# Kernel tuning notes

Measured on AMD Instinct MI355X. Metric: run time of the kernel, lower is better.

The kernel has to match this reference:

```python
import jax, jax.numpy as jnp
import numpy as np

N_NODES = 646  # fixed by nn.LayerNorm([646, 64])
LN_EPS = 1e-5


def gcn_conv(x, edge_index, W, b):
    """PyG GCNConv: out = D^-1/2 (A+I) D^-1/2 (x W) + b, scatter-add at target."""
    n = x.shape[0]
    h = x @ W  # [N, out_dim]
    loop = jnp.arange(n, dtype=edge_index.dtype)
    row = jnp.concatenate([edge_index[0], loop])  # source
    col = jnp.concatenate([edge_index[1], loop])  # target
    deg = jax.ops.segment_sum(jnp.ones_like(col, dtype=h.dtype), col, num_segments=n)
    dinv = jnp.where(deg > 0, jax.lax.rsqrt(deg), 0.0)
    norm = dinv[row] * dinv[col]  # [E+N]
    out = jax.ops.segment_sum(h[row] * norm[:, None], col, num_segments=n)
    return out + b


def setup_inputs() -> dict:
    key = jax.random.key(0)
    ks = jax.random.split(key, 8)
    F, H, L, E = 32768, 64, 128, 646 * 64
    x = jax.random.normal(ks[0], (N_NODES, F), dtype=jnp.float32)
    edge_index = jax.random.randint(ks[1], (2, E), 0, N_NODES, dtype=jnp.int64)
    s = 1.0 / np.sqrt(F)
    W1 = jax.random.normal(ks[2], (F, H), dtype=jnp.float32) * s
    b1 = jax.random.normal(ks[3], (H,), dtype=jnp.float32) * 0.01
    W2 = jax.random.normal(ks[4], (H, L), dtype=jnp.float32) * (1.0 / np.sqrt(H))
    b2 = jax.random.normal(ks[5], (L,), dtype=jnp.float32) * 0.01
    LPw = jax.random.normal(ks[6], (F, H), dtype=jnp.float32) * s
    LPb = jax.random.normal(ks[7], (H,), dtype=jnp.float32) * 0.01
    return {"x": x, "edge_index": edge_index, "W1": W1, "b1": b1,
            "W2": W2, "b2": b2, "LPw": LPw, "LPb": LPb}


def reference(x, edge_index, W1, b1, W2, b2, LPw, LPb):
    res = x @ LPw + LPb                       # Linear residual branch [N, 64]
    h = gcn_conv(x, edge_index, W1, b1)       # GCN1 [N, 64]
    h = res + h
    h = h * jax.nn.sigmoid(h)                 # SiLU
    # LayerNorm over BOTH dims [646, 64], no affine (elementwise_affine=False)
    mu = jnp.mean(h)
    var = jnp.mean(jnp.square(h - mu))
    h = (h - mu) * jax.lax.rsqrt(var + LN_EPS)
    out = gcn_conv(h, edge_index, W2, b2)     # GCN2 [N, num_label]
    return out
```

## Files before the change

kernel.cpp:

```cpp
#include <hip/hip_runtime.h>
#include <hip/hip_bf16.h>

#define NN 646
#define FF 32768
#define HH 64
#define LL 128
#define TOT (NN*HH)
#define OUTTOT (NN*LL)
#define WT_STRIDE (FF + 32)
#define KSPLIT 32
#define KSLICE (FF / KSPLIT)
#define NSTEP (KSLICE / 64)

typedef float f32x4 __attribute__((ext_vector_type(4)));
typedef short short8 __attribute__((ext_vector_type(8)));

__device__ __forceinline__ unsigned short f2bf(float f) {
  __hip_bfloat16 h = __float2bfloat16(f);
  return __builtin_bit_cast(unsigned short, h);
}
__device__ __forceinline__ short8 pack8(float4 u, float4 v) {
  short8 r;
  r[0] = (short)f2bf(u.x); r[1] = (short)f2bf(u.y);
  r[2] = (short)f2bf(u.z); r[3] = (short)f2bf(u.w);
  r[4] = (short)f2bf(v.x); r[5] = (short)f2bf(v.y);
  r[6] = (short)f2bf(v.z); r[7] = (short)f2bf(v.w);
  return r;
}
__device__ __forceinline__ void gload16(const void* g, void* l) {
  __builtin_amdgcn_global_load_lds(
      (const __attribute__((address_space(1))) void*)g,
      (__attribute__((address_space(3))) void*)l, 16, 0, 0);
}
__device__ __forceinline__ bool probe_i64(const int* e32, int* orr) {
  if (threadIdx.x == 0) *orr = 0;
  __syncthreads();
  if (threadIdx.x < 256 && e32[2 * threadIdx.x + 1] != 0) atomicOr(orr, 1);
  __syncthreads();
  return *orr == 0;
}

__global__ __launch_bounds__(256) void k_init(const float* __restrict__ W1,
                                              const float* __restrict__ LPw,
                                              unsigned short* __restrict__ wt,
                                              const int* __restrict__ e32, int E,
                                              int* __restrict__ cnt,
                                              const float* __restrict__ W2,
                                              float* __restrict__ cs) {
  if (blockIdx.x < 512) {
    __shared__ float t[64][129];
    int k0 = blockIdx.x * 64;
    for (int idx = threadIdx.x; idx < 64 * 128; idx += 256) {
      int kk = idx >> 7, n = idx & 127;
      float v = (n < 64) ? W1[(size_t)(k0 + kk) * 64 + n]
                         : LPw[(size_t)(k0 + kk) * 64 + (n - 64)];
      t[kk][n] = v;
    }
    __syncthreads();
    for (int idx = threadIdx.x; idx < 1024; idx += 256) {
      int n = idx >> 3;
      int kc = (idx & 7) * 8;
      short8 v;
#pragma unroll
      for (int u = 0; u < 8; ++u) v[u] = (short)f2bf(t[kc + u][n]);
      *reinterpret_cast<short8*>(&wt[(size_t)n * WT_STRIDE + k0 + kc]) = v;
    }
    return;
  }
  if (blockIdx.x == 576) {
    __shared__ float r2[2][128];
    int j = threadIdx.x & 127, h = threadIdx.x >> 7;
    float a = 0.f;
    for (int k = h * 32; k < h * 32 + 32; ++k) a += W2[k * LL + j];
    r2[h][j] = a;
    __syncthreads();
    if (h == 0) cs[j] = r2[0][j] + r2[1][j];
    return;
  }
  __shared__ int orr;
  bool i64 = probe_i64(e32, &orr);
  const int* cp = i64 ? (e32 + 2 * (size_t)E) : (e32 + E);
  int st = i64 ? 2 : 1;
  int wid = (blockIdx.x - 512) * 256 + threadIdx.x;
  for (int e = wid; e < E; e += 64 * 256)
    atomicAdd(&cnt[cp[(size_t)e * st]], 1);
}

__global__ __launch_bounds__(256, 3) void k_gemm(const float* __restrict__ x,
                                                 const unsigned short* __restrict__ wt,
                                                 float* __restrict__ partial,
                                                 const int* __restrict__ cnt, int E,
                                                 int* __restrict__ offsets,
                                                 float* __restrict__ dinv,
                                                 int* __restrict__ cursor) {
  __shared__ __align__(16) float As[2][32 * 64];
  __shared__ __align__(16) unsigned short Bs[2][128 * 64];

  int p = blockIdx.x;
  if (p == 672) {
    __shared__ int wtot[4];
    int tid = threadIdx.x;
    int b = 3 * tid;
    int c0 = (b < NN) ? cnt[b] : 0;
    int c1 = (b + 1 < NN) ? cnt[b + 1] : 0;
    int c2 = (b + 2 < NN) ? cnt[b + 2] : 0;
    int s = c0 + c1 + c2;
    int lane = tid & 63, wv = tid >> 6;
    int run = s;
#pragma unroll
    for (int o = 1; o < 64; o <<= 1) { int v = __shfl_up(run, o); if (lane >= o) run += v; }
    if (lane == 63) wtot[wv] = run;
    __syncthreads();
    int wbase = 0;
    for (int i = 0; i < wv; ++i) wbase += wtot[i];
    int excl = wbase + run - s;
    if (b < NN)     { offsets[b]     = excl;           cursor[b]     = excl;           dinv[b]     = rsqrtf((float)(c0 + 1)); }
    if (b + 1 < NN) { offsets[b + 1] = excl + c0;      cursor[b + 1] = excl + c0;      dinv[b + 1] = rsqrtf((float)(c1 + 1)); }
    if (b + 2 < NN) { offsets[b + 2] = excl + c0 + c1; cursor[b + 2] = excl + c0 + c1; dinv[b + 2] = rsqrtf((float)(c2 + 1)); }
    if (tid == 0) offsets[NN] = E;
    return;
  }

  int xcd = p & 7, idx = p >> 3;
  int ks = xcd + 8 * (idx / 21);
  int mt = idx % 21;
  int tid = threadIdx.x;
  int w = tid >> 6, l = tid & 63;
  int lr = l & 15, g = l >> 4;
  int mh = w & 1, nh = w >> 1;
  int ksbase = ks * KSLICE;

  f32x4 acc0 = {0.f, 0.f, 0.f, 0.f}, acc1 = acc0, acc2 = acc0, acc3 = acc0;
  int arow = mh * 16 + lr, arm = arow & 7;

  auto STAGE = [&](int buf, int step) {
    int kb = ksbase + step * 64;
#pragma unroll
    for (int j = 0; j < 2; ++j) {
      int pp = j * 256 + tid;
      int row = pp >> 4, cc = pp & 15;
      int c = cc ^ (row & 7);
      int rowg = mt * 32 + row; if (rowg > NN - 1) rowg = NN - 1;
      gload16(x + (size_t)rowg * FF + kb + c * 4, (char*)(&As[buf][0]) + pp * 16);
    }
#pragma unroll
    for (int j = 0; j < 4; ++j) {
      int pp = j * 256 + tid;
      int row = pp >> 3, cc = pp & 7;
      int c = cc ^ (row & 7);
      gload16(wt + (size_t)row * WT_STRIDE + kb + c * 8, (char*)(&Bs[buf][0]) + pp * 16);
    }
  };

  auto COMPUTE = [&](int buf) {
    const char* Ab = (const char*)(&As[buf][0]);
    const char* Bb = (const char*)(&Bs[buf][0]);
    int c0 = g * 2, c1 = 8 + g * 2;
    float4 lo0 = *(const float4*)(Ab + (arow * 16 + (c0 ^ arm)) * 16);
    float4 hi0 = *(const float4*)(Ab + (arow * 16 + ((c0 + 1) ^ arm)) * 16);
    float4 lo1 = *(const float4*)(Ab + (arow * 16 + (c1 ^ arm)) * 16);
    float4 hi1 = *(const float4*)(Ab + (arow * 16 + ((c1 + 1) ^ arm)) * 16);
    short8 af0 = pack8(lo0, hi0);
    short8 af1 = pack8(lo1, hi1);
#pragma unroll
    for (int nf = 0; nf < 4; ++nf) {
      int brow = nh * 64 + nf * 16 + lr;
      int brm = brow & 7;
      short8 b0 = *(const short8*)(Bb + (brow * 8 + (g ^ brm)) * 16);
      short8 b1 = *(const short8*)(Bb + (brow * 8 + ((4 + g) ^ brm)) * 16);
      f32x4* ac = (nf == 0) ? &acc0 : (nf == 1) ? &acc1 : (nf == 2) ? &acc2 : &acc3;
      *ac = __builtin_amdgcn_mfma_f32_16x16x32_bf16(af0, b0, *ac, 0, 0, 0);
      *ac = __builtin_amdgcn_mfma_f32_16x16x32_bf16(af1, b1, *ac, 0, 0, 0);
    }
  };

  STAGE(0, 0);
  STAGE(1, 1);
#pragma unroll
  for (int t = 0; t < NSTEP; ++t) {
    if (t + 1 < NSTEP) {
      asm volatile("s_waitcnt vmcnt(6)" ::: "memory");
    } else {
      asm volatile("s_waitcnt vmcnt(0)" ::: "memory");
    }
    __builtin_amdgcn_s_barrier();
    COMPUTE(t & 1);
    if (t + 2 < NSTEP) {
      __builtin_amdgcn_s_barrier();
      STAGE(t & 1, t + 2);
    }
  }

  float* pp = partial + (size_t)ks * OUTTOT;
  int colb = nh * 64 + lr;
#pragma unroll
  for (int j = 0; j < 4; ++j) {
    int m = mt * 32 + mh * 16 + g * 4 + j;
    if (m < NN) {
      pp[m * LL + colb]      = acc0[j];
      pp[m * LL + colb + 16] = acc1[j];
      pp[m * LL + colb + 32] = acc2[j];
      pp[m * LL + colb + 48] = acc3[j];
    }
  }
}

__global__ __launch_bounds__(256) void k_redplace(const float* __restrict__ partial,
                                                  const float* __restrict__ LPb,
                                                  float* __restrict__ hcat,
                                                  const int* __restrict__ e32, int E,
                                                  int* __restrict__ cursor,
                                                  int* __restrict__ srcs) {
  if (blockIdx.x < 81) {
    int i4 = blockIdx.x * 256 + threadIdx.x;
    if (i4 * 4 >= OUTTOT) return;
    f32x4 s = {0.f, 0.f, 0.f, 0.f};
#pragma unroll
    for (int ks = 0; ks < KSPLIT; ++ks)
      s += *reinterpret_cast<const f32x4*>(partial + (size_t)ks * OUTTOT + i4 * 4);
    int n = (i4 * 4) & 127;
    if (n & 64) s += *reinterpret_cast<const f32x4*>(LPb + (n - 64));
    *reinterpret_cast<f32x4*>(hcat + i4 * 4) = s;
    return;
  }
  __shared__ int orr;
  bool i64 = probe_i64(e32, &orr);
  int e = (blockIdx.x - 81) * 256 + threadIdx.x;
  if (e >= E) return;
  const int* rp = e32;
  const int* cp = i64 ? (e32 + 2 * (size_t)E) : (e32 + E);
  int st = i64 ? 2 : 1;
  int r = rp[(size_t)e * st];
  int c = cp[(size_t)e * st];
  int pos = atomicAdd(&cursor[c], 1);
  srcs[pos] = r;
}

__global__ __launch_bounds__(256) void k_fuse1(const int* __restrict__ offs,
                                               const int* __restrict__ srcs,
                                               const float* __restrict__ dinv,
                                               const float* __restrict__ hcat,
                                               const float* __restrict__ b1,
                                               const float* __restrict__ W2,
                                               float* __restrict__ hwr,
                                               float* __restrict__ sdi,
                                               float* __restrict__ stats) {
  int c = blockIdx.x;
  int j = threadIdx.x & 63, qt = threadIdx.x >> 6;
  int o0 = offs[c], o1 = offs[c + 1];
  float acc = 0.f, sd = 0.f;
  for (int i = o0 + qt; i < o1; i += 4) {
    int r = srcs[i];
    float dr = dinv[r];
    acc += hcat[r * LL + j] * dr;
    sd += dr;
  }
  __shared__ float red[4][64];
  __shared__ float sdl[4];
  __shared__ float hnl[64];
  red[qt][j] = acc;
  if (j == 0) sdl[qt] = sd;
  __syncthreads();
  if (qt == 0) {
    float di = dinv[c];
    float gb = (red[0][j] + red[1][j] + red[2][j] + red[3][j]) * di;
    float t = hcat[c * LL + 64 + j] + b1[j] + gb + hcat[c * LL + j] * di * di;
    float s = t / (1.f + __expf(-t));
    hnl[j] = s;
    float sum = s, sq = s * s;
#pragma unroll
    for (int o = 32; o; o >>= 1) { sum += __shfl_down(sum, o); sq += __shfl_down(sq, o); }
    if (j == 0) {
      atomicAdd(&stats[0], sum);
      atomicAdd(&stats[1], sq);
      sdi[c] = sdl[0] + sdl[1] + sdl[2] + sdl[3] + di;
    }
  }
  __syncthreads();
  int j2 = threadIdx.x & 127, h = threadIdx.x >> 7;
  float a2 = 0.f;
#pragma unroll
  for (int k = h * 32; k < h * 32 + 32; ++k) a2 += hnl[k] * W2[k * LL + j2];
  __shared__ float r2[2][128];
  r2[h][j2] = a2;
  __syncthreads();
  if (h == 0) hwr[c * LL + j2] = (r2[0][j2] + r2[1][j2]) * dinv[c];
}

__global__ __launch_bounds__(256) void k_fuse2(const int* __restrict__ offs,
                                               const int* __restrict__ srcs,
                                               const float* __restrict__ dinv,
                                               const float* __restrict__ hwr,
                                               const float* __restrict__ b2,
                                               const float* __restrict__ cs,
                                               const float* __restrict__ sdi,
                                               const float* __restrict__ stats,
                                               float* __restrict__ out) {
  int c = blockIdx.x;
  int j = threadIdx.x & 127, hf = threadIdx.x >> 7;
  int o0 = offs[c], o1 = offs[c + 1];
  float acc = 0.f;
  for (int i = o0 + hf; i < o1; i += 2) acc += hwr[srcs[i] * LL + j];
  __shared__ float red[2][128];
  red[hf][j] = acc;
  __syncthreads();
  if (hf == 0) {
    float mu = stats[0] * (1.f / TOT);
    float var = stats[1] * (1.f / TOT) - mu * mu;
    float rs = rsqrtf(var + 1e-5f);
    float S = red[0][j] + red[1][j] + hwr[c * LL + j];
    out[c * LL + j] = b2[j] + dinv[c] * (rs * S - rs * mu * cs[j] * sdi[c]);
  }
}

extern "C" void kernel_launch(void* const* d_in, const int* in_sizes, int n_in,
                              void* d_out, int out_size, void* d_ws, size_t ws_size,
                              hipStream_t stream) {
  const float* x   = (const float*)d_in[0];
  const int*   e32 = (const int*)d_in[1];
  const float* W1  = (const float*)d_in[2];
  const float* b1  = (const float*)d_in[3];
  const float* W2  = (const float*)d_in[4];
  const float* b2  = (const float*)d_in[5];
  const float* LPw = (const float*)d_in[6];
  const float* LPb = (const float*)d_in[7];
  int E = in_sizes[1] / 2;
  float* out = (float*)d_out;

  char* ws = (char*)d_ws;
  size_t o_wt      = 0;
  size_t o_partial = 8396800;
  size_t o_hcat    = o_partial + (size_t)KSPLIT * OUTTOT * 4;
  size_t o_hwr     = o_hcat + 330752;
  size_t o_dinv    = o_hwr + 330752;
  size_t o_offs    = o_dinv + 2816;
  size_t o_cnt     = o_offs + 2816;
  size_t o_stat    = o_cnt + 2592;
  size_t o_cur     = o_cnt + 2816;
  size_t o_srcs    = o_cur + 2816;
  size_t o_cs      = o_srcs + 165376;
  size_t o_sdi     = o_cs + 512;

  unsigned short* wt = (unsigned short*)(ws + o_wt);
  float* partial = (float*)(ws + o_partial);
  float* hcat    = (float*)(ws + o_hcat);
  float* hwr     = (float*)(ws + o_hwr);
  float* dinv    = (float*)(ws + o_dinv);
  int*   offs    = (int*)(ws + o_offs);
  int*   cnt     = (int*)(ws + o_cnt);
  float* stats   = (float*)(ws + o_stat);
  int*   cursor  = (int*)(ws + o_cur);
  int*   srcs    = (int*)(ws + o_srcs);
  float* cs      = (float*)(ws + o_cs);
  float* sdi     = (float*)(ws + o_sdi);

  hipMemsetAsync(ws + o_cnt, 0, 2600, stream);
  k_init<<<577, 256, 0, stream>>>(W1, LPw, wt, e32, E, cnt, W2, cs);
  k_gemm<<<673, 256, 0, stream>>>(x, wt, partial, cnt, E, offs, dinv, cursor);
  k_redplace<<<243, 256, 0, stream>>>(partial, LPb, hcat, e32, E, cursor, srcs);
  k_fuse1<<<NN, 256, 0, stream>>>(offs, srcs, dinv, hcat, b1, W2, hwr, sdi, stats);
  k_fuse2<<<NN, 256, 0, stream>>>(offs, srcs, dinv, hwr, b2, cs, sdi, stats, out);
}
```

Measured before the change: 97.56 us.

## Reschedule graph prep into init, overlap edge placement with GEMM, double K-split

Degree counting, the prefix scan and dinv/offset computation now run in a single k_init block using shared-memory atomics. This removes the memset, the global count array and the scan block in the GEMM. Edge placement into CSR moves out of the reduction kernel into extra blocks of the GEMM launch, so it overlaps the matmul. KSPLIT doubles to 64 for more GEMM blocks, which doubles the partial-sum buffer the reduction kernel must read. The single-block degree count over ~41k edges may become a serial tail in k_init.

```diff
diff --git a/kernel.cpp b/kernel.cpp
--- a/kernel.cpp
+++ b/kernel.cpp
@@ -8,9 +8,10 @@
 #define TOT (NN*HH)
 #define OUTTOT (NN*LL)
 #define WT_STRIDE (FF + 32)
-#define KSPLIT 32
+#define KSPLIT 64
 #define KSLICE (FF / KSPLIT)
 #define NSTEP (KSLICE / 64)
+#define NGEMM (21 * KSPLIT)
 
 typedef float f32x4 __attribute__((ext_vector_type(4)));
 typedef short short8 __attribute__((ext_vector_type(8)));
@@ -44,7 +45,10 @@
                                               const float* __restrict__ LPw,
                                               unsigned short* __restrict__ wt,
                                               const int* __restrict__ e32, int E,
-                                              int* __restrict__ cnt,
+                                              float* __restrict__ dinv,
+                                              int* __restrict__ offsets,
+                                              int* __restrict__ cursor,
+                                              float* __restrict__ stats,
                                               const float* __restrict__ W2,
                                               float* __restrict__ cs) {
   if (blockIdx.x < 512) {
@@ -67,7 +71,7 @@
     }
     return;
   }
-  if (blockIdx.x == 576) {
+  if (blockIdx.x == 513) {
     __shared__ float r2[2][128];
     int j = threadIdx.x & 127, h = threadIdx.x >> 7;
     float a = 0.f;
@@ -77,47 +81,59 @@
     if (h == 0) cs[j] = r2[0][j] + r2[1][j];
     return;
   }
+  __shared__ int cnt[648];
+  __shared__ int wtot[4];
   __shared__ int orr;
+  int tid = threadIdx.x;
+  if (tid < 2) stats[tid] = 0.f;
+  for (int i = tid; i < 648; i += 256) cnt[i] = 0;
   bool i64 = probe_i64(e32, &orr);
   const int* cp = i64 ? (e32 + 2 * (size_t)E) : (e32 + E);
   int st = i64 ? 2 : 1;
-  int wid = (blockIdx.x - 512) * 256 + threadIdx.x;
-  for (int e = wid; e < E; e += 64 * 256)
-    atomicAdd(&cnt[cp[(size_t)e * st]], 1);
+  for (int e = tid; e < E; e += 256) atomicAdd(&cnt[cp[(size_t)e * st]], 1);
+  __syncthreads();
+  int b = 3 * tid;
+  int c0 = (b < NN) ? cnt[b] : 0;
+  int c1 = (b + 1 < NN) ? cnt[b + 1] : 0;
+  int c2 = (b + 2 < NN) ? cnt[b + 2] : 0;
+  int s = c0 + c1 + c2;
+  int lane = tid & 63, wv = tid >> 6;
+  int run = s;
+#pragma unroll
+  for (int o = 1; o < 64; o <<= 1) { int v = __shfl_up(run, o); if (lane >= o) run += v; }
+  if (lane == 63) wtot[wv] = run;
+  __syncthreads();
+  int wbase = 0;
+  for (int i = 0; i < wv; ++i) wbase += wtot[i];
+  int excl = wbase + run - s;
+  if (b < NN)     { offsets[b]     = excl;           cursor[b]     = excl;           dinv[b]     = rsqrtf((float)(c0 + 1)); }
+  if (b + 1 < NN) { offsets[b + 1] = excl + c0;      cursor[b + 1] = excl + c0;      dinv[b + 1] = rsqrtf((float)(c1 + 1)); }
+  if (b + 2 < NN) { offsets[b + 2] = excl + c0 + c1; cursor[b + 2] = excl + c0 + c1; dinv[b + 2] = rsqrtf((float)(c2 + 1)); }
+  if (tid == 0) offsets[NN] = E;
 }
 
 __global__ __launch_bounds__(256, 3) void k_gemm(const float* __restrict__ x,
                                                  const unsigned short* __restrict__ wt,
                                                  float* __restrict__ partial,
-                                                 const int* __restrict__ cnt, int E,
-                                                 int* __restrict__ offsets,
-                                                 float* __restrict__ dinv,
-                                                 int* __restrict__ cursor) {
+                                                 const int* __restrict__ e32, int E,
+                                                 int* __restrict__ cursor,
+                                                 int* __restrict__ srcs) {
   __shared__ __align__(16) float As[2][32 * 64];
   __shared__ __align__(16) unsigned short Bs[2][128 * 64];
 
   int p = blockIdx.x;
-  if (p == 672) {
-    __shared__ int wtot[4];
-    int tid = threadIdx.x;
-    int b = 3 * tid;
-    int c0 = (b < NN) ? cnt[b] : 0;
-    int c1 = (b + 1 < NN) ? cnt[b + 1] : 0;
-    int c2 = (b + 2 < NN) ? cnt[b + 2] : 0;
-    int s = c0 + c1 + c2;
-    int lane = tid & 63, wv = tid >> 6;
-    int run = s;
-#pragma unroll
-    for (int o = 1; o < 64; o <<= 1) { int v = __shfl_up(run, o); if (lane >= o) run += v; }
-    if (lane == 63) wtot[wv] = run;
-    __syncthreads();
-    int wbase = 0;
-    for (int i = 0; i < wv; ++i) wbase += wtot[i];
-    int excl = wbase + run - s;
-    if (b < NN)     { offsets[b]     = excl;           cursor[b]     = excl;           dinv[b]     = rsqrtf((float)(c0 + 1)); }
-    if (b + 1 < NN) { offsets[b + 1] = excl + c0;      cursor[b + 1] = excl + c0;      dinv[b + 1] = rsqrtf((float)(c1 + 1)); }
-    if (b + 2 < NN) { offsets[b + 2] = excl + c0 + c1; cursor[b + 2] = excl + c0 + c1; dinv[b + 2] = rsqrtf((float)(c2 + 1)); }
-    if (tid == 0) offsets[NN] = E;
+  if (p >= NGEMM) {
+    __shared__ int orr;
+    bool i64 = probe_i64(e32, &orr);
+    int e = (p - NGEMM) * 256 + threadIdx.x;
+    if (e >= E) return;
+    const int* rp = e32;
+    const int* cp = i64 ? (e32 + 2 * (size_t)E) : (e32 + E);
+    int st = i64 ? 2 : 1;
+    int r = rp[(size_t)e * st];
+    int c = cp[(size_t)e * st];
+    int pos = atomicAdd(&cursor[c], 1);
+    srcs[pos] = r;
     return;
   }
 
@@ -205,35 +221,18 @@
   }
 }
 
-__global__ __launch_bounds__(256) void k_redplace(const float* __restrict__ partial,
-                                                  const float* __restrict__ LPb,
-                                                  float* __restrict__ hcat,
-                                                  const int* __restrict__ e32, int E,
-                                                  int* __restrict__ cursor,
-                                                  int* __restrict__ srcs) {
-  if (blockIdx.x < 81) {
-    int i4 = blockIdx.x * 256 + threadIdx.x;
-    if (i4 * 4 >= OUTTOT) return;
-    f32x4 s = {0.f, 0.f, 0.f, 0.f};
-#pragma unroll
-    for (int ks = 0; ks < KSPLIT; ++ks)
-      s += *reinterpret_cast<const f32x4*>(partial + (size_t)ks * OUTTOT + i4 * 4);
-    int n = (i4 * 4) & 127;
-    if (n & 64) s += *reinterpret_cast<const f32x4*>(LPb + (n - 64));
-    *reinterpret_cast<f32x4*>(hcat + i4 * 4) = s;
-    return;
-  }
-  __shared__ int orr;
-  bool i64 = probe_i64(e32, &orr);
-  int e = (blockIdx.x - 81) * 256 + threadIdx.x;
-  if (e >= E) return;
-  const int* rp = e32;
-  const int* cp = i64 ? (e32 + 2 * (size_t)E) : (e32 + E);
-  int st = i64 ? 2 : 1;
-  int r = rp[(size_t)e * st];
-  int c = cp[(size_t)e * st];
-  int pos = atomicAdd(&cursor[c], 1);
-  srcs[pos] = r;
+__global__ __launch_bounds__(256) void k_red(const float* __restrict__ partial,
+                                             const float* __restrict__ LPb,
+                                             float* __restrict__ hcat) {
+  int i4 = blockIdx.x * 256 + threadIdx.x;
+  if (i4 * 4 >= OUTTOT) return;
+  f32x4 s = {0.f, 0.f, 0.f, 0.f};
+#pragma unroll 8
+  for (int ks = 0; ks < KSPLIT; ++ks)
+    s += *reinterpret_cast<const f32x4*>(partial + (size_t)ks * OUTTOT + i4 * 4);
+  int n = (i4 * 4) & 127;
+  if (n & 64) s += *reinterpret_cast<const f32x4*>(LPb + (n - 64));
+  *reinterpret_cast<f32x4*>(hcat + i4 * 4) = s;
 }
 
 __global__ __launch_bounds__(256) void k_fuse1(const int* __restrict__ offs,
@@ -334,9 +333,8 @@
   size_t o_hwr     = o_hcat + 330752;
   size_t o_dinv    = o_hwr + 330752;
   size_t o_offs    = o_dinv + 2816;
-  size_t o_cnt     = o_offs + 2816;
-  size_t o_stat    = o_cnt + 2592;
-  size_t o_cur     = o_cnt + 2816;
+  size_t o_stat    = o_offs + 2816;
+  size_t o_cur     = o_stat + 256;
   size_t o_srcs    = o_cur + 2816;
   size_t o_cs      = o_srcs + 165376;
   size_t o_sdi     = o_cs + 512;
@@ -347,17 +345,16 @@
   float* hwr     = (float*)(ws + o_hwr);
   float* dinv    = (float*)(ws + o_dinv);
   int*   offs    = (int*)(ws + o_offs);
-  int*   cnt     = (int*)(ws + o_cnt);
   float* stats   = (float*)(ws + o_stat);
   int*   cursor  = (int*)(ws + o_cur);
   int*   srcs    = (int*)(ws + o_srcs);
   float* cs      = (float*)(ws + o_cs);
   float* sdi     = (float*)(ws + o_sdi);
 
-  hipMemsetAsync(ws + o_cnt, 0, 2600, stream);
-  k_init<<<577, 256, 0, stream>>>(W1, LPw, wt, e32, E, cnt, W2, cs);
-  k_gemm<<<673, 256, 0, stream>>>(x, wt, partial, cnt, E, offs, dinv, cursor);
-  k_redplace<<<243, 256, 0, stream>>>(partial, LPb, hcat, e32, E, cursor, srcs);
+  int nplace = (E + 255) / 256;
+  k_init<<<514, 256, 0, stream>>>(W1, LPw, wt, e32, E, dinv, offs, cursor, stats, W2, cs);
+  k_gemm<<<NGEMM + nplace, 256, 0, stream>>>(x, wt, partial, e32, E, cursor, srcs);
+  k_red<<<(OUTTOT / 4 + 255) / 256, 256, 0, stream>>>(partial, LPb, hcat);
   k_fuse1<<<NN, 256, 0, stream>>>(offs, srcs, dinv, hcat, b1, W2, hwr, sdi, stats);
   k_fuse2<<<NN, 256, 0, stream>>>(offs, srcs, dinv, hwr, b2, cs, sdi, stats, out);
 }
```

New measurement: 121.5 us, median of 6. +24.6%, slower.
